# Optimization experiments

Hardware: AMD Instinct MI355X
Metric: run time of the kernel (lower is better)

## Reference

```python
import jax, jax.numpy as jnp
import numpy as np

B, T, E = 4, 2048, 1024
H, D = 16, 64  # n_heads, head_size


def setup_inputs() -> dict:
    key = jax.random.key(0)
    ks = jax.random.split(key, 6)
    s = 0.02
    x = jax.random.normal(ks[0], (B, T, E), dtype=jnp.float32)
    Wq = jax.random.normal(ks[1], (H, E, D), dtype=jnp.float32) * s
    Wk = jax.random.normal(ks[2], (H, E, D), dtype=jnp.float32) * s
    Wv = jax.random.normal(ks[3], (H, E, D), dtype=jnp.float32) * s
    Wp = jax.random.normal(ks[4], (E, E), dtype=jnp.float32) * s
    bp = jnp.zeros((E,), dtype=jnp.float32)
    return {"x": x, "Wq": Wq, "Wk": Wk, "Wv": Wv, "Wp": Wp, "bp": bp}


def reference(x, Wq, Wk, Wv, Wp, bp):
    # Per-head bias-free Q/K/V projections (vectorized over heads)
    q = jnp.einsum('bte,hed->bhtd', x, Wq)
    k = jnp.einsum('bte,hed->bhtd', x, Wk)
    v = jnp.einsum('bte,hed->bhtd', x, Wv)
    scale = 1.0 / jnp.sqrt(jnp.asarray(D, dtype=x.dtype))
    scores = jnp.einsum('bhtd,bhsd->bhts', q, k) * scale  # [B,H,T,T]
    causal = jnp.tril(jnp.ones((T, T), dtype=bool))
    scores = jnp.where(causal, scores, jnp.asarray(-jnp.inf, dtype=scores.dtype))
    attn = jax.nn.softmax(scores, axis=-1)
    out = jnp.einsum('bhts,bhsd->bhtd', attn, v)  # [B,H,T,D]
    # concat heads: 'nh b t c -> b t (nh c)'
    out = out.transpose(0, 2, 1, 3).reshape(B, T, H * D)
    # output projection (dropout p=0.0 is identity)
    return out @ Wp.T + bp
```

## Files before the change

kernel.cpp:

```cpp
#include <hip/hip_runtime.h>

typedef unsigned short u16;
typedef __attribute__((ext_vector_type(8))) short bf16x8;
typedef __attribute__((ext_vector_type(4))) short bf16x4;
typedef __attribute__((ext_vector_type(4))) float f32x4;

__device__ __forceinline__ u16 f2bf(float f) {
  unsigned u = __float_as_uint(f);
  u += 0x7FFFu + ((u >> 16) & 1u);
  return (u16)(u >> 16);
}
__device__ __forceinline__ unsigned pack2(float a, float b) {
  return (unsigned)f2bf(a) | ((unsigned)f2bf(b) << 16);
}
#if __has_builtin(__builtin_amdgcn_cvt_pk_bf16_f32)
typedef __attribute__((ext_vector_type(2))) __bf16 bf16v2;
__device__ __forceinline__ unsigned cvt_pk(float a, float b) {
  bf16v2 v = __builtin_amdgcn_cvt_pk_bf16_f32(a, b);
  return __builtin_bit_cast(unsigned, v);
}
#else
__device__ __forceinline__ unsigned cvt_pk(float a, float b) { return pack2(a, b); }
#endif
__device__ __forceinline__ uint4 pack8(float4 a, float4 b) {
  uint4 r;
  r.x = pack2(a.x, a.y); r.y = pack2(a.z, a.w);
  r.z = pack2(b.x, b.y); r.w = pack2(b.z, b.w);
  return r;
}
__device__ __forceinline__ void gload16(const void* g, void* l) {
  __builtin_amdgcn_global_load_lds(
      (const __attribute__((address_space(1))) void*)g,
      (__attribute__((address_space(3))) void*)l, 16, 0, 0);
}
__device__ __forceinline__ f32x4 mfma16(bf16x4 a, bf16x4 b, f32x4 c) {
#if __has_builtin(__builtin_amdgcn_mfma_f32_16x16x16bf16_1k)
  return __builtin_amdgcn_mfma_f32_16x16x16bf16_1k(a, b, c, 0, 0, 0);
#elif __has_builtin(__builtin_amdgcn_mfma_f32_16x16x16_bf16)
  return __builtin_amdgcn_mfma_f32_16x16x16_bf16(a, b, c, 0, 0, 0);
#else
  asm volatile("v_mfma_f32_16x16x16_bf16 %0, %1, %2, %0\n\ts_nop 2"
               : "+v"(c) : "v"(a), "v"(b));
  return c;
#endif
}

__global__ __launch_bounds__(256) void prep(
    const float* __restrict__ x, u16* __restrict__ xbf,
    const float* __restrict__ Wq, const float* __restrict__ Wk,
    const float* __restrict__ Wv, u16* __restrict__ wt,
    const float* __restrict__ Wp, u16* __restrict__ wpbf) {
  const int tid = threadIdx.x;
  const int b = blockIdx.x;
  __shared__ __align__(16) u16 tile[64 * 72];
  if (b < 4096) {
    const size_t i = (size_t)b * 256 + tid;
    const float4* p = (const float4*)(x + i * 8);
    *(uint4*)(xbf + i * 8) = pack8(p[0], p[1]);
  } else if (b < 4864) {
    const int idx = b - 4096;
    const int w = idx >> 8;
    const int mat = (idx >> 4) & 15;
    const int r0 = (idx & 15) * 64;
    const float* src = (w == 0 ? Wq : (w == 1 ? Wk : Wv)) + (size_t)mat * 1024 * 64;
    u16* dst = wt + (size_t)w * 1024 * 1024 + (size_t)mat * 1024 * 64;
#pragma unroll
    for (int i = 0; i < 2; ++i) {
      const int c = tid + i * 256;
      const int r = c >> 3, off = (c & 7) * 8;
      const float* p = src + (size_t)(r0 + r) * 64 + off;
      *(uint4*)(&tile[r * 72 + off]) = pack8(*(const float4*)p, *(const float4*)(p + 4));
    }
    __syncthreads();
#pragma unroll
    for (int i = 0; i < 2; ++i) {
      const int c = tid + i * 256;
      const int d = c >> 3, roff = (c & 7) * 8;
      bf16x8 v;
#pragma unroll
      for (int j = 0; j < 8; ++j) v[j] = (short)tile[(roff + j) * 72 + d];
      *(bf16x8*)(dst + (size_t)d * 1024 + r0 + roff) = v;
    }
  } else {
    const size_t i = (size_t)(b - 4864) * 256 + tid;
    const float4* p = (const float4*)(Wp + i * 8);
    *(uint4*)(wpbf + i * 8) = pack8(p[0], p[1]);
  }
}

template <int MODE>
__global__ __launch_bounds__(256) void gemm_bt(
    const u16* __restrict__ A, const u16* __restrict__ BT,
    u16* __restrict__ o0, u16* __restrict__ o1, u16* __restrict__ o2,
    float* __restrict__ fout, const float* __restrict__ bp) {
  __shared__ __align__(16) u16 As[128 * 32];
  __shared__ __align__(16) u16 Bs[128 * 32];
  const int tid = threadIdx.x;
  const int lane = tid & 63, wv = tid >> 6;
  const int g = lane >> 4, ln = lane & 15;
  const int wm = wv >> 1, wn = wv & 1;
  const int m0 = blockIdx.x * 128, n0 = blockIdx.y * 128;

  const f32x4 fz = {0.f, 0.f, 0.f, 0.f};
  f32x4 acc[4][4];
#pragma unroll
  for (int i = 0; i < 4; ++i)
#pragma unroll
    for (int j = 0; j < 4; ++j) acc[i][j] = fz;

  for (int k0 = 0; k0 < 1024; k0 += 32) {
    __syncthreads();
#pragma unroll
    for (int i = 0; i < 2; ++i) {
      const int c = tid + i * 256;
      const int r = c >> 2, off = (c & 3) * 8;
      gload16(A + (size_t)(m0 + r) * 1024 + k0 + off, &As[c * 8]);
      gload16(BT + (size_t)(n0 + r) * 1024 + k0 + off, &Bs[c * 8]);
    }
    __syncthreads();
    bf16x8 af[4], bfr[4];
#pragma unroll
    for (int rt = 0; rt < 4; ++rt)
      af[rt] = *(const bf16x8*)(&As[(wm * 64 + rt * 16 + ln) * 32 + g * 8]);
#pragma unroll
    for (int ct = 0; ct < 4; ++ct)
      bfr[ct] = *(const bf16x8*)(&Bs[(wn * 64 + ct * 16 + ln) * 32 + g * 8]);
#pragma unroll
    for (int rt = 0; rt < 4; ++rt)
#pragma unroll
      for (int ct = 0; ct < 4; ++ct)
        acc[rt][ct] = __builtin_amdgcn_mfma_f32_16x16x32_bf16(af[rt], bfr[ct],
                                                              acc[rt][ct], 0, 0, 0);
  }

  if (MODE == 0) {
    const int which = n0 >> 10;
    const int nl0 = (n0 & 1023) + wn * 64;
    const float qs = (which == 0) ? 0.1803368801f : 1.0f;
    if (which < 2) {
      u16* outp = which == 0 ? o0 : o1;
#pragma unroll
      for (int rt = 0; rt < 4; ++rt)
#pragma unroll
        for (int ct = 0; ct < 4; ++ct) {
          const int nl = nl0 + ct * 16 + ln;
          const int h = nl >> 6, d = nl & 63;
#pragma unroll
          for (int r = 0; r < 4; ++r) {
            const int m = m0 + wm * 64 + rt * 16 + 4 * g + r;
            const int b = m >> 11, t = m & 2047;
            outp[(((size_t)(b * 16 + h) * 2048 + t) << 6) + d] =
                f2bf(acc[rt][ct][r] * qs);
          }
        }
    } else {
#pragma unroll
      for (int rt = 0; rt < 4; ++rt) {
        const int tb = m0 + wm * 64 + rt * 16 + 4 * g;
        const int b = tb >> 11, t = tb & 2047;
#pragma unroll
        for (int ct = 0; ct < 4; ++ct) {
          const int nl = nl0 + ct * 16 + ln;
          const int h = nl >> 6, d = nl & 63;
          u16* dst = o2 + ((size_t)((b * 16 + h) * 64 + d) << 11) + t;
#pragma unroll
          for (int r = 0; r < 4; ++r) dst[r] = f2bf(acc[rt][ct][r]);
        }
      }
    }
  } else {
#pragma unroll
    for (int ct = 0; ct < 4; ++ct) {
      const int n = n0 + wn * 64 + ct * 16 + ln;
      const float bias = bp[n];
#pragma unroll
      for (int rt = 0; rt < 4; ++rt)
#pragma unroll
        for (int r = 0; r < 4; ++r) {
          const int m = m0 + wm * 64 + rt * 16 + 4 * g + r;
          fout[(size_t)m * 1024 + n] = acc[rt][ct][r] + bias;
        }
    }
  }
}

__global__ __launch_bounds__(256) void attn_kernel(
    const u16* __restrict__ Q, const u16* __restrict__ K,
    const u16* __restrict__ VT, u16* __restrict__ AO) {
  const int tid = threadIdx.x;
  const int wv = tid >> 6, lane = tid & 63, g = lane >> 4, ln = lane & 15;
  const int bh = blockIdx.x;
  const int jb = blockIdx.y;
  const u16* Qb = Q + (size_t)bh * (2048 * 64);
  const u16* Kb = K + (size_t)bh * (2048 * 64);
  const u16* Vb = VT + (size_t)bh * (64 * 2048);

  __shared__ __align__(16) u16 Ks[64 * 72];
  __shared__ __align__(16) u16 Vs[64 * 72];

  const int sr0 = tid >> 3, so0 = (tid & 7) * 8;
  const int sr1 = sr0 + 32;

  uint4 kpf0 = *(const uint4*)(Kb + (size_t)sr0 * 64 + so0);
  uint4 kpf1 = *(const uint4*)(Kb + (size_t)sr1 * 64 + so0);
  uint4 vpf0 = *(const uint4*)(Vb + (size_t)sr0 * 2048 + so0);
  uint4 vpf1 = *(const uint4*)(Vb + (size_t)sr1 * 2048 + so0);

  const int b = bh >> 4, h = bh & 15;
  const short ob = 0x3F80;
  const bf16x4 ones = {ob, ob, ob, ob};
  const f32x4 fz = {0.f, 0.f, 0.f, 0.f};

#pragma unroll
  for (int ph = 0; ph < 2; ++ph) {
    const int qi = (ph == 0) ? jb : 15 - jb;
    const int q0 = qi * 128;
    const int nt = 2 * qi + 2;
    const int ntw = 2 * qi + 1 + (wv >> 1);

    bf16x8 qa[2][2];
#pragma unroll
    for (int rt = 0; rt < 2; ++rt) {
      const int row = q0 + wv * 32 + rt * 16 + ln;
#pragma unroll
      for (int hh = 0; hh < 2; ++hh)
        qa[rt][hh] = *(const bf16x8*)(Qb + (size_t)row * 64 + hh * 32 + g * 8);
    }

    f32x4 oacc[2][4], lacc[2];
#pragma unroll
    for (int rt = 0; rt < 2; ++rt) {
      lacc[rt] = fz;
#pragma unroll
      for (int dt = 0; dt < 4; ++dt) oacc[rt][dt] = fz;
    }

    for (int kt = 0; kt < nt; ++kt) {
      __syncthreads();
      *(uint4*)(&Ks[sr0 * 72 + so0]) = kpf0;
      *(uint4*)(&Ks[sr1 * 72 + so0]) = kpf1;
      *(uint4*)(&Vs[sr0 * 72 + so0]) = vpf0;
      *(uint4*)(&Vs[sr1 * 72 + so0]) = vpf1;
      __syncthreads();
      if ((kt + 1 < nt) || (ph == 0)) {
        const int sn = (kt + 1 < nt) ? (kt + 1) * 64 : 0;
        kpf0 = *(const uint4*)(Kb + (size_t)(sn + sr0) * 64 + so0);
        kpf1 = *(const uint4*)(Kb + (size_t)(sn + sr1) * 64 + so0);
        vpf0 = *(const uint4*)(Vb + (size_t)sr0 * 2048 + sn + so0);
        vpf1 = *(const uint4*)(Vb + (size_t)sr1 * 2048 + sn + so0);
      }
      if (kt < ntw) {
        const int s0 = kt * 64;
        f32x4 sfT[2][4];
#pragma unroll
        for (int rt = 0; rt < 2; ++rt)
#pragma unroll
          for (int st = 0; st < 4; ++st) sfT[rt][st] = fz;
#pragma unroll
        for (int st = 0; st < 4; ++st) {
          const bf16x8 kb0 = *(const bf16x8*)(&Ks[(st * 16 + ln) * 72 + g * 8]);
          const bf16x8 kb1 = *(const bf16x8*)(&Ks[(st * 16 + ln) * 72 + 32 + g * 8]);
#pragma unroll
          for (int rt = 0; rt < 2; ++rt) {
            sfT[rt][st] = __builtin_amdgcn_mfma_f32_16x16x32_bf16(kb0, qa[rt][0],
                                                                  sfT[rt][st], 0, 0, 0);
            sfT[rt][st] = __builtin_amdgcn_mfma_f32_16x16x32_bf16(kb1, qa[rt][1],
                                                                  sfT[rt][st], 0, 0, 0);
          }
        }
        const bool diag = (kt == ntw - 1);
        bf16x4 pa[2][4];
#pragma unroll
        for (int rt = 0; rt < 2; ++rt) {
          const int qloc = wv * 32 + rt * 16 + ln;
#pragma unroll
          for (int st = 0; st < 4; ++st) {
            float e[4];
#pragma unroll
            for (int r = 0; r < 4; ++r) e[r] = __builtin_amdgcn_exp2f(sfT[rt][st][r]);
            if (diag) {
              const int sloc = s0 - q0 + st * 16 + 4 * g;
#pragma unroll
              for (int r = 0; r < 4; ++r)
                if (sloc + r > qloc) e[r] = 0.f;
            }
            uint2 packed = {cvt_pk(e[0], e[1]), cvt_pk(e[2], e[3])};
            pa[rt][st] = __builtin_bit_cast(bf16x4, packed);
          }
        }
#pragma unroll
        for (int st = 0; st < 4; ++st) {
#pragma unroll
          for (int dt = 0; dt < 4; ++dt) {
            const bf16x4 vb =
                *(const bf16x4*)(&Vs[(dt * 16 + ln) * 72 + st * 16 + 4 * g]);
#pragma unroll
            for (int rt = 0; rt < 2; ++rt)
              oacc[rt][dt] = mfma16(pa[rt][st], vb, oacc[rt][dt]);
          }
#pragma unroll
          for (int rt = 0; rt < 2; ++rt)
            lacc[rt] = mfma16(pa[rt][st], ones, lacc[rt]);
        }
      }
    }
#pragma unroll
    for (int rt = 0; rt < 2; ++rt) {
      float linv[4];
#pragma unroll
      for (int r = 0; r < 4; ++r) linv[r] = 1.f / lacc[rt][r];
#pragma unroll
      for (int dt = 0; dt < 4; ++dt)
#pragma unroll
        for (int r = 0; r < 4; ++r) {
          const int qg = q0 + wv * 32 + rt * 16 + 4 * g + r;
          AO[(size_t)(b * 2048 + qg) * 1024 + h * 64 + dt * 16 + ln] =
              f2bf(oacc[rt][dt][r] * linv[r]);
        }
    }
  }
}

extern "C" void kernel_launch(void* const* d_in, const int* in_sizes, int n_in,
                              void* d_out, int out_size, void* d_ws, size_t ws_size,
                              hipStream_t stream) {
  const float* x  = (const float*)d_in[0];
  const float* Wq = (const float*)d_in[1];
  const float* Wk = (const float*)d_in[2];
  const float* Wv = (const float*)d_in[3];
  const float* Wp = (const float*)d_in[4];
  const float* bp = (const float*)d_in[5];
  float* out = (float*)d_out;

  char* ws = (char*)d_ws;
  const size_t MB = 1048576;
  u16* xbf  = (u16*)(ws);
  u16* aows = (u16*)(ws);
  u16* wt   = (u16*)(ws + 16 * MB);
  u16* wpbf = (u16*)(ws + 22 * MB);
  u16* qws  = (u16*)(ws + 24 * MB);
  u16* kws  = (u16*)(ws + 40 * MB);
  u16* vtws = (u16*)(ws + 56 * MB);

  prep<<<dim3(5376), 256, 0, stream>>>(x, xbf, Wq, Wk, Wv, wt, Wp, wpbf);
  gemm_bt<0><<<dim3(64, 24), 256, 0, stream>>>(xbf, wt, qws, kws, vtws,
                                               nullptr, nullptr);
  attn_kernel<<<dim3(64, 8), 256, 0, stream>>>(qws, kws, vtws, aows);
  gemm_bt<1><<<dim3(64, 8), 256, 0, stream>>>(aows, wpbf, nullptr, nullptr,
                                              nullptr, out, bp);
}
```

Before: 268.2 us.

## Double-buffer K/V shared tiles in attention and use packed bf16 conversion

The attention loop now uses two LDS buffers for K and V. Each step writes the next tile while computing on the current one, which drops one of the two barriers per step. Global prefetch now runs two tiles ahead and continues seamlessly across both query phases. Separately, bf16 rounding in the GEMM epilogues and the attention output switches to the hardware packed convert, and V-transpose stores become 8-byte vector stores. LDS use doubles, which may affect occupancy.

```diff
diff --git a/kernel.cpp b/kernel.cpp
--- a/kernel.cpp
+++ b/kernel.cpp
@@ -24,8 +24,8 @@
 #endif
 __device__ __forceinline__ uint4 pack8(float4 a, float4 b) {
   uint4 r;
-  r.x = pack2(a.x, a.y); r.y = pack2(a.z, a.w);
-  r.z = pack2(b.x, b.y); r.w = pack2(b.z, b.w);
+  r.x = cvt_pk(a.x, a.y); r.y = cvt_pk(a.z, a.w);
+  r.z = cvt_pk(b.x, b.y); r.w = cvt_pk(b.z, b.w);
   return r;
 }
 __device__ __forceinline__ void gload16(const void* g, void* l) {
@@ -145,12 +145,14 @@
         for (int ct = 0; ct < 4; ++ct) {
           const int nl = nl0 + ct * 16 + ln;
           const int h = nl >> 6, d = nl & 63;
+          const unsigned p01 = cvt_pk(acc[rt][ct][0] * qs, acc[rt][ct][1] * qs);
+          const unsigned p23 = cvt_pk(acc[rt][ct][2] * qs, acc[rt][ct][3] * qs);
+          const u16 vv[4] = {(u16)p01, (u16)(p01 >> 16), (u16)p23, (u16)(p23 >> 16)};
 #pragma unroll
           for (int r = 0; r < 4; ++r) {
             const int m = m0 + wm * 64 + rt * 16 + 4 * g + r;
             const int b = m >> 11, t = m & 2047;
-            outp[(((size_t)(b * 16 + h) * 2048 + t) << 6) + d] =
-                f2bf(acc[rt][ct][r] * qs);
+            outp[(((size_t)(b * 16 + h) * 2048 + t) << 6) + d] = vv[r];
           }
         }
     } else {
@@ -162,9 +164,10 @@
         for (int ct = 0; ct < 4; ++ct) {
           const int nl = nl0 + ct * 16 + ln;
           const int h = nl >> 6, d = nl & 63;
-          u16* dst = o2 + ((size_t)((b * 16 + h) * 64 + d) << 11) + t;
-#pragma unroll
-          for (int r = 0; r < 4; ++r) dst[r] = f2bf(acc[rt][ct][r]);
+          uint2 pv;
+          pv.x = cvt_pk(acc[rt][ct][0], acc[rt][ct][1]);
+          pv.y = cvt_pk(acc[rt][ct][2], acc[rt][ct][3]);
+          *(uint2*)(o2 + ((size_t)((b * 16 + h) * 64 + d) << 11) + t) = pv;
         }
       }
     }
@@ -195,21 +198,102 @@
   const u16* Kb = K + (size_t)bh * (2048 * 64);
   const u16* Vb = VT + (size_t)bh * (64 * 2048);
 
-  __shared__ __align__(16) u16 Ks[64 * 72];
-  __shared__ __align__(16) u16 Vs[64 * 72];
+  __shared__ __align__(16) u16 Ks[2][64 * 72];
+  __shared__ __align__(16) u16 Vs[2][64 * 72];
 
   const int sr0 = tid >> 3, so0 = (tid & 7) * 8;
-  const int sr1 = sr0 + 32;
-
-  uint4 kpf0 = *(const uint4*)(Kb + (size_t)sr0 * 64 + so0);
-  uint4 kpf1 = *(const uint4*)(Kb + (size_t)sr1 * 64 + so0);
-  uint4 vpf0 = *(const uint4*)(Vb + (size_t)sr0 * 2048 + so0);
-  uint4 vpf1 = *(const uint4*)(Vb + (size_t)sr1 * 2048 + so0);
+  const int wK0 = sr0 * 72 + so0, wK1 = (sr0 + 32) * 72 + so0;
+  const size_t lK0 = (size_t)sr0 * 64 + so0, lK1 = (size_t)(sr0 + 32) * 64 + so0;
+  const size_t lV0 = (size_t)sr0 * 2048 + so0, lV1 = (size_t)(sr0 + 32) * 2048 + so0;
+
+  const int ntA = 2 * jb + 2;
+
+  uint4 kpf0 = *(const uint4*)(Kb + lK0);
+  uint4 kpf1 = *(const uint4*)(Kb + lK1);
+  uint4 vpf0 = *(const uint4*)(Vb + lV0);
+  uint4 vpf1 = *(const uint4*)(Vb + lV1);
+  *(uint4*)(&Ks[0][wK0]) = kpf0;
+  *(uint4*)(&Ks[0][wK1]) = kpf1;
+  *(uint4*)(&Vs[0][wK0]) = vpf0;
+  *(uint4*)(&Vs[0][wK1]) = vpf1;
+  {
+    const int s1 = (1 < ntA ? 1 : 1 - ntA) * 64;
+    kpf0 = *(const uint4*)(Kb + (size_t)s1 * 64 + lK0);
+    kpf1 = *(const uint4*)(Kb + (size_t)s1 * 64 + lK1);
+    vpf0 = *(const uint4*)(Vb + s1 + lV0);
+    vpf1 = *(const uint4*)(Vb + s1 + lV1);
+  }
 
   const int b = bh >> 4, h = bh & 15;
   const short ob = 0x3F80;
   const bf16x4 ones = {ob, ob, ob, ob};
   const f32x4 fz = {0.f, 0.f, 0.f, 0.f};
+  int gbase = 0;
+
+#define ATTN_STEP(KT, BB)                                                      \
+  {                                                                            \
+    __syncthreads();                                                           \
+    const int g1 = gbase + (KT) + 1;                                           \
+    if (g1 < 34) {                           \
+      *(uint4*)(&Ks[(BB) ^ 1][wK0]) = kpf0;                                    \
+      *(uint4*)(&Ks[(BB) ^ 1][wK1]) = kpf1;                                    \
+      *(uint4*)(&Vs[(BB) ^ 1][wK0]) = vpf0;                                    \
+      *(uint4*)(&Vs[(BB) ^ 1][wK1]) = vpf1;                                    \
+    }                                                                          \
+    const int g2 = gbase + (KT) + 2;                                           \
+    if (g2 < 34) {                            \
+      const int sn = (g2 < ntA ? g2 : g2 - ntA) * 64;                          \
+      kpf0 = *(const uint4*)(Kb + (size_t)sn * 64 + lK0);                      \
+      kpf1 = *(const uint4*)(Kb + (size_t)sn * 64 + lK1);                      \
+      vpf0 = *(const uint4*)(Vb + sn + lV0);                                   \
+      vpf1 = *(const uint4*)(Vb + sn + lV1);                                   \
+    }                                                                          \
+    if ((KT) < ntw) {                                                          \
+      f32x4 sfT[2][4];                                                         \
+      _Pragma("unroll") for (int rt = 0; rt < 2; ++rt)                         \
+          _Pragma("unroll") for (int st = 0; st < 4; ++st) sfT[rt][st] = fz;   \
+      _Pragma("unroll") for (int st = 0; st < 4; ++st) {                       \
+        const bf16x8 kb0 =                                                     \
+            *(const bf16x8*)(&Ks[BB][(st * 16 + ln) * 72 + g * 8]);            \
+        const bf16x8 kb1 =                                                     \
+            *(const bf16x8*)(&Ks[BB][(st * 16 + ln) * 72 + 32 + g * 8]);       \
+        _Pragma("unroll") for (int rt = 0; rt < 2; ++rt) {                     \
+          sfT[rt][st] = __builtin_amdgcn_mfma_f32_16x16x32_bf16(               \
+              kb0, qa[rt][0], sfT[rt][st], 0, 0, 0);                           \
+          sfT[rt][st] = __builtin_amdgcn_mfma_f32_16x16x32_bf16(               \
+              kb1, qa[rt][1], sfT[rt][st], 0, 0, 0);                           \
+        }                                                                      \
+      }                                                                        \
+      const bool diag = ((KT) == ntw - 1);                                     \
+      const int s0q = (KT)*64 - q0;                                            \
+      bf16x4 pa[2][4];                                                         \
+      _Pragma("unroll") for (int rt = 0; rt < 2; ++rt) {                       \
+        const int qloc = wv * 32 + rt * 16 + ln;                               \
+        _Pragma("unroll") for (int st = 0; st < 4; ++st) {                     \
+          float e[4];                                                          \
+          _Pragma("unroll") for (int r = 0; r < 4; ++r)                        \
+              e[r] = __builtin_amdgcn_exp2f(sfT[rt][st][r]);                   \
+          if (diag) {                                                          \
+            const int sloc = s0q + st * 16 + 4 * g;                            \
+            _Pragma("unroll") for (int r = 0; r < 4; ++r)                      \
+                if (sloc + r > qloc) e[r] = 0.f;                               \
+          }                                                                    \
+          uint2 packed = {cvt_pk(e[0], e[1]), cvt_pk(e[2], e[3])};             \
+          pa[rt][st] = __builtin_bit_cast(bf16x4, packed);                     \
+        }                                                                      \
+      }                                                                        \
+      _Pragma("unroll") for (int st = 0; st < 4; ++st) {                       \
+        _Pragma("unroll") for (int dt = 0; dt < 4; ++dt) {                     \
+          const bf16x4 vb = *(const bf16x4*)(                                  \
+              &Vs[BB][(dt * 16 + ln) * 72 + st * 16 + 4 * g]);                 \
+          _Pragma("unroll") for (int rt = 0; rt < 2; ++rt)                     \
+              oacc[rt][dt] = mfma16(pa[rt][st], vb, oacc[rt][dt]);             \
+        }                                                                      \
+        _Pragma("unroll") for (int rt = 0; rt < 2; ++rt)                       \
+            lacc[rt] = mfma16(pa[rt][st], ones, lacc[rt]);                     \
+      }                                                                        \
+    }                                                                          \
+  }
 
 #pragma unroll
   for (int ph = 0; ph < 2; ++ph) {
@@ -226,7 +310,6 @@
       for (int hh = 0; hh < 2; ++hh)
         qa[rt][hh] = *(const bf16x8*)(Qb + (size_t)row * 64 + hh * 32 + g * 8);
     }
-
     f32x4 oacc[2][4], lacc[2];
 #pragma unroll
     for (int rt = 0; rt < 2; ++rt) {
@@ -235,90 +318,33 @@
       for (int dt = 0; dt < 4; ++dt) oacc[rt][dt] = fz;
     }
 
-    for (int kt = 0; kt < nt; ++kt) {
-      __syncthreads();
-      *(uint4*)(&Ks[sr0 * 72 + so0]) = kpf0;
-      *(uint4*)(&Ks[sr1 * 72 + so0]) = kpf1;
-      *(uint4*)(&Vs[sr0 * 72 + so0]) = vpf0;
-      *(uint4*)(&Vs[sr1 * 72 + so0]) = vpf1;
-      __syncthreads();
-      if ((kt + 1 < nt) || (ph == 0)) {
-        const int sn = (kt + 1 < nt) ? (kt + 1) * 64 : 0;
-        kpf0 = *(const uint4*)(Kb + (size_t)(sn + sr0) * 64 + so0);
-        kpf1 = *(const uint4*)(Kb + (size_t)(sn + sr1) * 64 + so0);
-        vpf0 = *(const uint4*)(Vb + (size_t)sr0 * 2048 + sn + so0);
-        vpf1 = *(const uint4*)(Vb + (size_t)sr1 * 2048 + sn + so0);
-      }
-      if (kt < ntw) {
-        const int s0 = kt * 64;
-        f32x4 sfT[2][4];
-#pragma unroll
-        for (int rt = 0; rt < 2; ++rt)
-#pragma unroll
-          for (int st = 0; st < 4; ++st) sfT[rt][st] = fz;
-#pragma unroll
-        for (int st = 0; st < 4; ++st) {
-          const bf16x8 kb0 = *(const bf16x8*)(&Ks[(st * 16 + ln) * 72 + g * 8]);
-          const bf16x8 kb1 = *(const bf16x8*)(&Ks[(st * 16 + ln) * 72 + 32 + g * 8]);
-#pragma unroll
-          for (int rt = 0; rt < 2; ++rt) {
-            sfT[rt][st] = __builtin_amdgcn_mfma_f32_16x16x32_bf16(kb0, qa[rt][0],
-                                                                  sfT[rt][st], 0, 0, 0);
-            sfT[rt][st] = __builtin_amdgcn_mfma_f32_16x16x32_bf16(kb1, qa[rt][1],
-                                                                  sfT[rt][st], 0, 0, 0);
-          }
-        }
-        const bool diag = (kt == ntw - 1);
-        bf16x4 pa[2][4];
-#pragma unroll
-        for (int rt = 0; rt < 2; ++rt) {
-          const int qloc = wv * 32 + rt * 16 + ln;
-#pragma unroll
-          for (int st = 0; st < 4; ++st) {
-            float e[4];
-#pragma unroll
-            for (int r = 0; r < 4; ++r) e[r] = __builtin_amdgcn_exp2f(sfT[rt][st][r]);
-            if (diag) {
-              const int sloc = s0 - q0 + st * 16 + 4 * g;
-#pragma unroll
-              for (int r = 0; r < 4; ++r)
-                if (sloc + r > qloc) e[r] = 0.f;
-            }
-            uint2 packed = {cvt_pk(e[0], e[1]), cvt_pk(e[2], e[3])};
-            pa[rt][st] = __builtin_bit_cast(bf16x4, packed);
-          }
-        }
-#pragma unroll
-        for (int st = 0; st < 4; ++st) {
-#pragma unroll
-          for (int dt = 0; dt < 4; ++dt) {
-            const bf16x4 vb =
-                *(const bf16x4*)(&Vs[(dt * 16 + ln) * 72 + st * 16 + 4 * g]);
-#pragma unroll
-            for (int rt = 0; rt < 2; ++rt)
-              oacc[rt][dt] = mfma16(pa[rt][st], vb, oacc[rt][dt]);
-          }
-#pragma unroll
-          for (int rt = 0; rt < 2; ++rt)
-            lacc[rt] = mfma16(pa[rt][st], ones, lacc[rt]);
+    for (int kt = 0; kt < nt; kt += 2) {
+      ATTN_STEP(kt, 0);
+      ATTN_STEP(kt + 1, 1);
+    }
+    gbase += nt;
+
+#pragma unroll
+    for (int rt = 0; rt < 2; ++rt) {
+      float linv[4];
+#pragma unroll
+      for (int r = 0; r < 4; ++r) linv[r] = 1.f / lacc[rt][r];
+#pragma unroll
+      for (int dt = 0; dt < 4; ++dt) {
+        const unsigned p01 =
+            cvt_pk(oacc[rt][dt][0] * linv[0], oacc[rt][dt][1] * linv[1]);
+        const unsigned p23 =
+            cvt_pk(oacc[rt][dt][2] * linv[2], oacc[rt][dt][3] * linv[3]);
+        const u16 vv[4] = {(u16)p01, (u16)(p01 >> 16), (u16)p23, (u16)(p23 >> 16)};
+#pragma unroll
+        for (int r = 0; r < 4; ++r) {
+          const int qg = q0 + wv * 32 + rt * 16 + 4 * g + r;
+          AO[(size_t)(b * 2048 + qg) * 1024 + h * 64 + dt * 16 + ln] = vv[r];
         }
       }
     }
-#pragma unroll
-    for (int rt = 0; rt < 2; ++rt) {
-      float linv[4];
-#pragma unroll
-      for (int r = 0; r < 4; ++r) linv[r] = 1.f / lacc[rt][r];
-#pragma unroll
-      for (int dt = 0; dt < 4; ++dt)
-#pragma unroll
-        for (int r = 0; r < 4; ++r) {
-          const int qg = q0 + wv * 32 + rt * 16 + 4 * g + r;
-          AO[(size_t)(b * 2048 + qg) * 1024 + h * 64 + dt * 16 + ln] =
-              f2bf(oacc[rt][dt][r] * linv[r]);
-        }
-    }
-  }
+  }
+#undef ATTN_STEP
 }
 
 extern "C" void kernel_launch(void* const* d_in, const int* in_sizes, int n_in,
```

New measurement: 266.9 us. No clear change (-0.5%).
